# Kernel optimization log

Measured on AMD Instinct MI355X. Metric: run time of the kernel, lower is better.

The kernel has to match this reference:

```python
import jax, jax.numpy as jnp
import numpy as np

N_EMBD = 1024
N_HEAD = 16
HEAD_SIZE = N_EMBD // N_HEAD


def setup_inputs() -> dict:
    key = jax.random.key(0)
    k1, k2, k3, k4 = jax.random.split(key, 4)
    x = jax.random.normal(k1, (2, 2048, N_EMBD), dtype=jnp.float32)
    # nn.Linear weights: stored as [out, in]; apply as x @ W.T
    scale = 1.0 / np.sqrt(N_EMBD)
    W_kqv = jax.random.uniform(k2, (3 * N_EMBD, N_EMBD), jnp.float32, -scale, scale)
    W_proj = jax.random.uniform(k3, (N_EMBD, N_EMBD), jnp.float32, -scale, scale)
    b_proj = jax.random.uniform(k4, (N_EMBD,), jnp.float32, -scale, scale)
    return {"x": x, "W_kqv": W_kqv, "W_proj": W_proj, "b_proj": b_proj}


def reference(x, W_kqv, W_proj, b_proj):
    B, T, C = x.shape
    H, D = N_HEAD, HEAD_SIZE
    kqv = x @ W_kqv.T  # [B, T, 3C]
    # source splits as k, q, v (k first)
    k, q, v = jnp.split(kqv, 3, axis=-1)
    k = k.reshape(B, T, H, D).transpose(0, 2, 1, 3)  # [B,H,T,D]
    q = q.reshape(B, T, H, D).transpose(0, 2, 1, 3)
    v = v.reshape(B, T, H, D).transpose(0, 2, 1, 3)
    wei = jnp.einsum('bhqd,bhkd->bhqk', q, k) * (D ** -0.5)  # [B,H,T,T]
    causal = jnp.tril(jnp.ones((T, T), dtype=bool))
    wei = jnp.where(causal[None, None], wei, -jnp.inf)
    wei = jax.nn.softmax(wei, axis=-1)
    out = jnp.einsum('bhqk,bhkd->bhqd', wei, v)  # [B,H,T,D]
    out = out.transpose(0, 2, 1, 3).reshape(B, T, C)
    return out @ W_proj.T + b_proj
```

## Files before the change

### kernel.cpp

```cpp
#include <hip/hip_runtime.h>
#include <cstdint>


typedef __bf16 bf16x8 __attribute__((ext_vector_type(8)));
typedef unsigned short u16x8 __attribute__((ext_vector_type(8)));
typedef float f32x4 __attribute__((ext_vector_type(4)));

__device__ __forceinline__ float bf2f(unsigned short u) {
    return __uint_as_float(((unsigned int)u) << 16);
}
__device__ __forceinline__ unsigned short f2bf(float f) {
    unsigned int u = __float_as_uint(f);
    u += 0x7fffu + ((u >> 16) & 1u);
    return (unsigned short)(u >> 16);
}
__device__ __forceinline__ void stC(float* p, float v) { *p = v; }
__device__ __forceinline__ void stC(unsigned short* p, float v) { *p = f2bf(v); }

__device__ __forceinline__ void gl2lds16(const unsigned short* g, unsigned short* l) {
    __builtin_amdgcn_global_load_lds(
        (__attribute__((address_space(1))) void*)g,
        (__attribute__((address_space(3))) void*)l, 16, 0, 0);
}

__device__ __forceinline__ unsigned short* swz(unsigned short* base, int row, int col) {
    const int off = ((row << 7) + (col << 1)) ^ ((row & 7) << 4);
    return (unsigned short*)((char*)base + off);
}
__device__ __forceinline__ const unsigned short* swz(const unsigned short* base, int row, int col) {
    const int off = ((row << 7) + (col << 1)) ^ ((row & 7) << 4);
    return (const unsigned short*)((const char*)base + off);
}

__device__ __forceinline__ void cvt8(const float* __restrict__ s, unsigned short* __restrict__ d) {
    const f32x4 a = *(const f32x4*)s;
    const f32x4 b = *(const f32x4*)(s + 4);
    u16x8 o;
    o[0] = f2bf(a[0]); o[1] = f2bf(a[1]); o[2] = f2bf(a[2]); o[3] = f2bf(a[3]);
    o[4] = f2bf(b[0]); o[5] = f2bf(b[1]); o[6] = f2bf(b[2]); o[7] = f2bf(b[3]);
    *(u16x8*)d = o;
}
__global__ __launch_bounds__(256) void cvt_bf16_3(
    const float* __restrict__ s0, unsigned short* __restrict__ d0, int n0,
    const float* __restrict__ s1, unsigned short* __restrict__ d1, int n1,
    const float* __restrict__ s2, unsigned short* __restrict__ d2, int n2)
{
    const int t = blockIdx.x * 256 + threadIdx.x;
    const int S = gridDim.x * 256;
    for (int i = t; i < n0 / 8; i += S) cvt8(s0 + (size_t)i * 8, d0 + (size_t)i * 8);
    for (int i = t; i < n1 / 8; i += S) cvt8(s1 + (size_t)i * 8, d1 + (size_t)i * 8);
    for (int i = t; i < n2 / 8; i += S) cvt8(s2 + (size_t)i * 8, d2 + (size_t)i * 8);
}

template <int P>
__device__ __forceinline__ void mfmaq(f32x4 (&acc)[8][4],
                                      const bf16x8 (&af)[2][2],
                                      const bf16x8 (&bfr)[4][2]) {
#pragma unroll
    for (int m2 = 0; m2 < 2; m2++)
#pragma unroll
        for (int nt = 0; nt < 4; nt++)
#pragma unroll
            for (int ks = 0; ks < 2; ks++)
                acc[2 * P + m2][nt] = __builtin_amdgcn_mfma_f32_16x16x32_bf16(
                    af[m2][ks], bfr[nt][ks], acc[2 * P + m2][nt], 0, 0, 0);
}

__global__ __launch_bounds__(512) void gemm_qkv(
    const unsigned short* __restrict__ A, const unsigned short* __restrict__ B,
    unsigned short* __restrict__ C, int M, int N, int K)
{
    __shared__ __align__(16) unsigned short As[2][256 * 64];
    __shared__ __align__(16) unsigned short Bs[2][256 * 64];

    const int tid = threadIdx.x;
    const int bn = blockIdx.x, bm = blockIdx.y;
    const int w = tid >> 6, lane = tid & 63;
    const int quad = lane >> 4, l16 = lane & 15;
    const int wm = (w >> 2) * 128, wn = (w & 3) * 64;
    const int NT = K >> 6;

    f32x4 acc[8][4] = {};

    const int srow8 = lane >> 3;
    const int scol = ((lane & 7) ^ srow8) * 8;
    const unsigned short* Ab = A + (size_t)bm * 256 * K;
    const unsigned short* Bb = B + (size_t)bn * 256 * K;

    auto stage = [&](const unsigned short* __restrict__ G, unsigned short* lds,
                     int tT, int hh) {
#pragma unroll
        for (int i = 0; i < 2; i++) {
            const int r = hh * 128 + w * 16 + i * 8;
            gl2lds16(G + (size_t)(r + srow8) * K + tT * 64 + scol, lds + r * 64);
        }
    };
    auto ldA = [&](bf16x8 (&af)[2][2], const unsigned short* AsB, int p) {
#pragma unroll
        for (int m2 = 0; m2 < 2; m2++)
#pragma unroll
            for (int ks = 0; ks < 2; ks++)
                af[m2][ks] = *(const bf16x8*)swz(AsB, wm + p * 32 + m2 * 16 + l16,
                                                 ks * 32 + quad * 8);
    };
    auto ldB = [&](bf16x8 (&bf_)[4][2], const unsigned short* BsB) {
#pragma unroll
        for (int nt = 0; nt < 4; nt++)
#pragma unroll
            for (int ks = 0; ks < 2; ks++)
                bf_[nt][ks] = *(const bf16x8*)swz(BsB, wn + nt * 16 + l16,
                                                  ks * 32 + quad * 8);
    };

    stage(Bb, Bs[0], 0, 0); stage(Bb, Bs[0], 0, 1);
    stage(Ab, As[0], 0, 0); stage(Ab, As[0], 0, 1);
    stage(Bb, Bs[1], 1, 0); stage(Bb, Bs[1], 1, 1);
    asm volatile("s_waitcnt vmcnt(4)" ::: "memory");
    __builtin_amdgcn_s_barrier();

    for (int t = 0; t < NT; t++) {
        const unsigned short* AsB = As[t & 1];
        const unsigned short* BsB = Bs[t & 1];
        unsigned short* AsN = As[(t + 1) & 1];
        unsigned short* BsN = Bs[t & 1];
        bf16x8 bfr[4][2];
        {
            bf16x8 af[2][2];
            ldA(af, AsB, 0);
            ldB(bfr, BsB);
            if (t + 1 < NT) stage(Ab, AsN, t + 1, 0);
            __builtin_amdgcn_s_barrier();
            asm volatile("s_waitcnt lgkmcnt(0)" ::: "memory");
            __builtin_amdgcn_sched_barrier(0);
            mfmaq<0>(acc, af, bfr);
            __builtin_amdgcn_s_barrier();
        }
        {
            bf16x8 af[2][2];
            ldA(af, AsB, 1);
            if (t + 1 < NT) stage(Ab, AsN, t + 1, 1);
            if (t + 2 < NT) stage(Bb, BsN, t + 2, 0);
            __builtin_amdgcn_s_barrier();
            asm volatile("s_waitcnt lgkmcnt(0)" ::: "memory");
            __builtin_amdgcn_sched_barrier(0);
            mfmaq<1>(acc, af, bfr);
            __builtin_amdgcn_s_barrier();
        }
        {
            bf16x8 af[2][2];
            ldA(af, AsB, 2);
            if (t + 2 < NT) stage(Bb, BsN, t + 2, 1);
            __builtin_amdgcn_s_barrier();
            asm volatile("s_waitcnt lgkmcnt(0)" ::: "memory");
            __builtin_amdgcn_sched_barrier(0);
            mfmaq<2>(acc, af, bfr);
            __builtin_amdgcn_s_barrier();
        }
        {
            bf16x8 af[2][2];
            ldA(af, AsB, 3);
            if (t < NT - 2)       asm volatile("s_waitcnt vmcnt(4)" ::: "memory");
            else if (t == NT - 2) asm volatile("s_waitcnt vmcnt(0)" ::: "memory");
            __builtin_amdgcn_s_barrier();
            asm volatile("s_waitcnt lgkmcnt(0)" ::: "memory");
            __builtin_amdgcn_sched_barrier(0);
            mfmaq<3>(acc, af, bfr);
            __builtin_amdgcn_s_barrier();
        }
    }

#pragma unroll
    for (int mf = 0; mf < 8; mf++) {
        const int row = bm * 256 + wm + mf * 16 + quad * 4;
#pragma unroll
        for (int nt = 0; nt < 4; nt++) {
            const int col = bn * 256 + wn + nt * 16 + l16;
#pragma unroll
            for (int r = 0; r < 4; r++)
                C[(size_t)(row + r) * N + col] = f2bf(acc[mf][nt][r]);
        }
    }
}

__global__ __launch_bounds__(256) void gemm_proj(
    const unsigned short* __restrict__ A, const unsigned short* __restrict__ B,
    const float* __restrict__ bias, float* __restrict__ C, int M, int N, int K)
{
    __shared__ __align__(16) unsigned short As[64 * 32];
    __shared__ __align__(16) unsigned short Bs[128 * 32];

    const int tid = threadIdx.x;
    const int bn = blockIdx.x, bm = blockIdx.y;
    const int w = tid >> 6, lane = tid & 63;
    const int quad = lane >> 4, l16 = lane & 15;
    const int wm = (w >> 1) * 32, wn = (w & 1) * 64;

    f32x4 acc[2][4] = {};

    const int srow = w * 16 + (lane >> 2);
    const int scol = (lane & 3) * 8;
    const unsigned short* Ag = &A[(size_t)(bm * 64 + srow) * K + scol];
    const unsigned short* Bg = &B[(size_t)(bn * 128 + srow) * K + scol];
    unsigned short* AsW = &As[(w * 16) * 32];
    unsigned short* BsW = &Bs[(w * 16) * 32];

    for (int k0 = 0; k0 < K; k0 += 32) {
        gl2lds16(Ag + k0, AsW);
        gl2lds16(Bg + k0, BsW);
        gl2lds16(Bg + (size_t)64 * K + k0, BsW + 64 * 32);
        __syncthreads();

        bf16x8 af[2], bfr[4];
#pragma unroll
        for (int t = 0; t < 2; t++)
            af[t]  = *(const bf16x8*)&As[(wm + t * 16 + l16) * 32 + quad * 8];
#pragma unroll
        for (int t = 0; t < 4; t++)
            bfr[t] = *(const bf16x8*)&Bs[(wn + t * 16 + l16) * 32 + quad * 8];
#pragma unroll
        for (int mt = 0; mt < 2; mt++)
#pragma unroll
            for (int nt = 0; nt < 4; nt++)
                acc[mt][nt] = __builtin_amdgcn_mfma_f32_16x16x32_bf16(
                    af[mt], bfr[nt], acc[mt][nt], 0, 0, 0);
        __syncthreads();
    }

#pragma unroll
    for (int mt = 0; mt < 2; mt++) {
        const int row = bm * 64 + wm + mt * 16 + quad * 4;
#pragma unroll
        for (int nt = 0; nt < 4; nt++) {
            const int col = bn * 128 + wn + nt * 16 + l16;
            const float bv = bias[col];
#pragma unroll
            for (int r = 0; r < 4; r++)
                C[(size_t)(row + r) * N + col] = acc[mt][nt][r] + bv;
        }
    }
}

__global__ __launch_bounds__(256) void attn_fused(
    const unsigned short* __restrict__ kqv,
    unsigned short* __restrict__ out)
{
    __shared__ __align__(16) unsigned short Qs[64 * 64];
    __shared__ __align__(16) unsigned short Ks[2][64 * 64];
    __shared__ __align__(16) unsigned short Vts[2][64 * 64];
    __shared__ __align__(16) unsigned short Ps[64 * 64];

    const int bh = blockIdx.x;
    const int qt = 31 - (int)blockIdx.y;
    const int b = bh >> 4, h = bh & 15;
    const int tid = threadIdx.x;
    const int w = tid >> 6;
    const int lane = tid & 63;
    const int quad = lane >> 4, l16 = lane & 15;
    const int rowBase = b * 2048;
    const int kOff = h * 64, qOff = 1024 + h * 64, vOff = 2048 + h * 64;
    const float SEXP = 0.125f * 1.4426950408889634f;
    const float MASKV = -1.0e30f;

#pragma unroll
    for (int i = 0; i < 2; i++) {
        const int v = tid + i * 256;
        const int row = v >> 3, c8 = (v & 7) * 8;
        *(u16x8*)swz(Qs, row, c8) =
            *(const u16x8*)&kqv[(size_t)(rowBase + qt * 64 + row) * 3072 + qOff + c8];
    }

    f32x4 o[4] = {};
    float l_i[4] = {0.f, 0.f, 0.f, 0.f};

    u16x8 kr[2], vr[2];
#pragma unroll
    for (int i = 0; i < 2; i++) {
        const int v = tid + i * 256;
        kr[i] = *(const u16x8*)&kqv[(size_t)(rowBase + (v >> 3)) * 3072 + kOff + (v & 7) * 8];
        vr[i] = *(const u16x8*)&kqv[(size_t)(rowBase + lane) * 3072 + vOff + (i * 4 + w) * 8];
    }

    for (int j = 0; j <= qt; j++) {
        const int cur = j & 1;
#pragma unroll
        for (int i = 0; i < 2; i++) {
            const int v = tid + i * 256;
            *(u16x8*)swz(Ks[cur], v >> 3, (v & 7) * 8) = kr[i];
            const int d8 = i * 4 + w;
#pragma unroll
            for (int u = 0; u < 8; u++)
                *swz(Vts[cur], d8 * 8 + u, lane) = vr[i][u];
        }
        __syncthreads();

        if (j < qt) {
#pragma unroll
            for (int i = 0; i < 2; i++) {
                const int v = tid + i * 256;
                kr[i] = *(const u16x8*)&kqv[(size_t)(rowBase + (j + 1) * 64 + (v >> 3)) * 3072 + kOff + (v & 7) * 8];
                vr[i] = *(const u16x8*)&kqv[(size_t)(rowBase + (j + 1) * 64 + lane) * 3072 + vOff + (i * 4 + w) * 8];
            }
        }

        f32x4 s[4] = {};
#pragma unroll
        for (int ks = 0; ks < 2; ks++) {
            const bf16x8 aq = *(const bf16x8*)swz(Qs, w * 16 + l16, ks * 32 + quad * 8);
#pragma unroll
            for (int nt = 0; nt < 4; nt++) {
                const bf16x8 bk = *(const bf16x8*)swz(Ks[cur], nt * 16 + l16, ks * 32 + quad * 8);
                s[nt] = __builtin_amdgcn_mfma_f32_16x16x32_bf16(aq, bk, s[nt], 0, 0, 0);
            }
        }

        if (j == qt) {
            const int rowl = w * 16 + quad * 4;
#pragma unroll
            for (int nt = 0; nt < 4; nt++) {
                const int coll = nt * 16 + l16;
#pragma unroll
                for (int r = 0; r < 4; r++)
                    if (coll > rowl + r) s[nt][r] = MASKV;
            }
        }

#pragma unroll
        for (int nt = 0; nt < 4; nt++) {
#pragma unroll
            for (int r = 0; r < 4; r++) {
                const float p = exp2f(s[nt][r] * SEXP);
                l_i[r] += p;
                *swz(Ps, w * 16 + quad * 4 + r, nt * 16 + l16) = f2bf(p);
            }
        }
        __syncthreads();

#pragma unroll
        for (int ks = 0; ks < 2; ks++) {
            const bf16x8 ap = *(const bf16x8*)swz(Ps, w * 16 + l16, ks * 32 + quad * 8);
#pragma unroll
            for (int nt = 0; nt < 4; nt++) {
                const bf16x8 bv = *(const bf16x8*)swz(Vts[cur], nt * 16 + l16, ks * 32 + quad * 8);
                o[nt] = __builtin_amdgcn_mfma_f32_16x16x32_bf16(ap, bv, o[nt], 0, 0, 0);
            }
        }
    }

    float linv[4];
#pragma unroll
    for (int r = 0; r < 4; r++) {
        float t = l_i[r];
        t += __shfl_xor(t, 1);
        t += __shfl_xor(t, 2);
        t += __shfl_xor(t, 4);
        t += __shfl_xor(t, 8);
        linv[r] = 1.0f / t;
    }

#pragma unroll
    for (int nt = 0; nt < 4; nt++) {
        const int col = h * 64 + nt * 16 + l16;
#pragma unroll
        for (int r = 0; r < 4; r++)
            out[(size_t)(rowBase + qt * 64 + w * 16 + quad * 4 + r) * 1024 + col] =
                f2bf(o[nt][r] * linv[r]);
    }
}

extern "C" void kernel_launch(void* const* d_in, const int* in_sizes, int n_in,
                              void* d_out, int out_size, void* d_ws, size_t ws_size,
                              hipStream_t stream) {
    const float* x     = (const float*)d_in[0];
    const float* Wkqv  = (const float*)d_in[1];
    const float* Wproj = (const float*)d_in[2];
    const float* bproj = (const float*)d_in[3];
    float* out = (float*)d_out;

    unsigned short* kqv    = (unsigned short*)d_ws;
    unsigned short* attn   = kqv    + (size_t)4096 * 3072;
    unsigned short* xb     = attn   + (size_t)4096 * 1024;
    unsigned short* wkqvb  = xb     + (size_t)4096 * 1024;
    unsigned short* wprojb = wkqvb  + (size_t)3072 * 1024;

    cvt_bf16_3<<<dim3(512), dim3(256), 0, stream>>>(
        x, xb, 4096 * 1024, Wkqv, wkqvb, 3072 * 1024, Wproj, wprojb, 1024 * 1024);

    gemm_qkv<<<dim3(12, 16), dim3(512), 0, stream>>>(
        xb, wkqvb, kqv, 4096, 3072, 1024);

    attn_fused<<<dim3(32, 32), dim3(256), 0, stream>>>(kqv, attn);

    gemm_proj<<<dim3(8, 64), dim3(256), 0, stream>>>(
        attn, wprojb, bproj, out, 4096, 1024, 1024);
}
```

Baseline: 182.9 us.

## Widen proj GEMM K-tile with swizzled LDS, prescale Q, use pointer increments

The projection GEMM now stages 64-wide K slices, loaded with an XOR-swizzled column pattern into LDS and read back through swz. This halves the number of barrier pairs per K sweep and is meant to reduce LDS bank conflicts. In attention, Q is prescaled by the softmax scale and log2(e) when loaded, which removes a multiply per score element. K/V load addresses are now advanced by pointer increments instead of recomputed each step. Prescaling Q and rounding it back to bf16 adds a small precision change.

After: 180.2 us. About the same (-1.4%).

```diff
diff --git a/kernel.cpp b/kernel.cpp
--- a/kernel.cpp
+++ b/kernel.cpp
@@ -186,8 +186,8 @@
     const unsigned short* __restrict__ A, const unsigned short* __restrict__ B,
     const float* __restrict__ bias, float* __restrict__ C, int M, int N, int K)
 {
-    __shared__ __align__(16) unsigned short As[64 * 32];
-    __shared__ __align__(16) unsigned short Bs[128 * 32];
+    __shared__ __align__(16) unsigned short As[64 * 64];
+    __shared__ __align__(16) unsigned short Bs[128 * 64];
 
     const int tid = threadIdx.x;
     const int bn = blockIdx.x, bm = blockIdx.y;
@@ -197,32 +197,38 @@
 
     f32x4 acc[2][4] = {};
 
-    const int srow = w * 16 + (lane >> 2);
-    const int scol = (lane & 3) * 8;
-    const unsigned short* Ag = &A[(size_t)(bm * 64 + srow) * K + scol];
-    const unsigned short* Bg = &B[(size_t)(bn * 128 + srow) * K + scol];
-    unsigned short* AsW = &As[(w * 16) * 32];
-    unsigned short* BsW = &Bs[(w * 16) * 32];
-
-    for (int k0 = 0; k0 < K; k0 += 32) {
-        gl2lds16(Ag + k0, AsW);
-        gl2lds16(Bg + k0, BsW);
-        gl2lds16(Bg + (size_t)64 * K + k0, BsW + 64 * 32);
+    const int srow8 = lane >> 3;
+    const int scol = ((lane & 7) ^ srow8) * 8;
+    const unsigned short* Ag = &A[(size_t)(bm * 64 + w * 16 + srow8) * K + scol];
+    const unsigned short* Bg = &B[(size_t)(bn * 128 + w * 32 + srow8) * K + scol];
+    unsigned short* AsW = &As[(w * 16) * 64];
+    unsigned short* BsW = &Bs[(w * 32) * 64];
+
+    for (int k0 = 0; k0 < K; k0 += 64) {
+#pragma unroll
+        for (int i = 0; i < 2; i++)
+            gl2lds16(Ag + (size_t)(i * 8) * K + k0, AsW + i * 8 * 64);
+#pragma unroll
+        for (int i = 0; i < 4; i++)
+            gl2lds16(Bg + (size_t)(i * 8) * K + k0, BsW + i * 8 * 64);
         __syncthreads();
 
-        bf16x8 af[2], bfr[4];
-#pragma unroll
-        for (int t = 0; t < 2; t++)
-            af[t]  = *(const bf16x8*)&As[(wm + t * 16 + l16) * 32 + quad * 8];
-#pragma unroll
-        for (int t = 0; t < 4; t++)
-            bfr[t] = *(const bf16x8*)&Bs[(wn + t * 16 + l16) * 32 + quad * 8];
-#pragma unroll
-        for (int mt = 0; mt < 2; mt++)
-#pragma unroll
-            for (int nt = 0; nt < 4; nt++)
-                acc[mt][nt] = __builtin_amdgcn_mfma_f32_16x16x32_bf16(
-                    af[mt], bfr[nt], acc[mt][nt], 0, 0, 0);
+#pragma unroll
+        for (int ks = 0; ks < 2; ks++) {
+            bf16x8 af[2], bfr[4];
+#pragma unroll
+            for (int t = 0; t < 2; t++)
+                af[t]  = *(const bf16x8*)swz(As, wm + t * 16 + l16, ks * 32 + quad * 8);
+#pragma unroll
+            for (int t = 0; t < 4; t++)
+                bfr[t] = *(const bf16x8*)swz(Bs, wn + t * 16 + l16, ks * 32 + quad * 8);
+#pragma unroll
+            for (int mt = 0; mt < 2; mt++)
+#pragma unroll
+                for (int nt = 0; nt < 4; nt++)
+                    acc[mt][nt] = __builtin_amdgcn_mfma_f32_16x16x32_bf16(
+                        af[mt], bfr[nt], acc[mt][nt], 0, 0, 0);
+        }
         __syncthreads();
     }
 
@@ -265,20 +271,26 @@
     for (int i = 0; i < 2; i++) {
         const int v = tid + i * 256;
         const int row = v >> 3, c8 = (v & 7) * 8;
-        *(u16x8*)swz(Qs, row, c8) =
+        const u16x8 raw =
             *(const u16x8*)&kqv[(size_t)(rowBase + qt * 64 + row) * 3072 + qOff + c8];
+        u16x8 sc;
+#pragma unroll
+        for (int e = 0; e < 8; e++) sc[e] = f2bf(bf2f(raw[e]) * SEXP);
+        *(u16x8*)swz(Qs, row, c8) = sc;
     }
 
     f32x4 o[4] = {};
     float l_i[4] = {0.f, 0.f, 0.f, 0.f};
 
+    const ptrdiff_t KV = (ptrdiff_t)64 * 3072;
+    const unsigned short* kp0 = &kqv[(size_t)(rowBase + (tid >> 3)) * 3072 + kOff + (tid & 7) * 8];
+    const unsigned short* kp1 = kp0 + (ptrdiff_t)32 * 3072;
+    const unsigned short* vp0 = &kqv[(size_t)(rowBase + lane) * 3072 + vOff + w * 8];
+    const unsigned short* vp1 = vp0 + 32;
+
     u16x8 kr[2], vr[2];
-#pragma unroll
-    for (int i = 0; i < 2; i++) {
-        const int v = tid + i * 256;
-        kr[i] = *(const u16x8*)&kqv[(size_t)(rowBase + (v >> 3)) * 3072 + kOff + (v & 7) * 8];
-        vr[i] = *(const u16x8*)&kqv[(size_t)(rowBase + lane) * 3072 + vOff + (i * 4 + w) * 8];
-    }
+    kr[0] = *(const u16x8*)kp0;  kr[1] = *(const u16x8*)kp1;
+    vr[0] = *(const u16x8*)vp0;  vr[1] = *(const u16x8*)vp1;
 
     for (int j = 0; j <= qt; j++) {
         const int cur = j & 1;
@@ -294,12 +306,9 @@
         __syncthreads();
 
         if (j < qt) {
-#pragma unroll
-            for (int i = 0; i < 2; i++) {
-                const int v = tid + i * 256;
-                kr[i] = *(const u16x8*)&kqv[(size_t)(rowBase + (j + 1) * 64 + (v >> 3)) * 3072 + kOff + (v & 7) * 8];
-                vr[i] = *(const u16x8*)&kqv[(size_t)(rowBase + (j + 1) * 64 + lane) * 3072 + vOff + (i * 4 + w) * 8];
-            }
+            kp0 += KV; kp1 += KV; vp0 += KV; vp1 += KV;
+            kr[0] = *(const u16x8*)kp0;  kr[1] = *(const u16x8*)kp1;
+            vr[0] = *(const u16x8*)vp0;  vr[1] = *(const u16x8*)vp1;
         }
 
         f32x4 s[4] = {};
@@ -328,7 +337,7 @@
         for (int nt = 0; nt < 4; nt++) {
 #pragma unroll
             for (int r = 0; r < 4; r++) {
-                const float p = exp2f(s[nt][r] * SEXP);
+                const float p = exp2f(s[nt][r]);
                 l_i[r] += p;
                 *swz(Ps, w * 16 + quad * 4 + r, nt * 16 + l16) = f2bf(p);
             }
```
